# Kernel optimization log

Hardware: AMD Instinct MI355X
Metric: run time of the kernel (lower is better)

Reference implementation:

```python
import jax, jax.numpy as jnp
from jax import lax
import numpy as np

KSIZE = 25  # kernel_size init arg


def _generate_kernel(size):
    center = size // 2
    kernel = np.zeros((size, size), dtype=np.float32)
    for i in range(size):
        if i < center + 1:
            for j in range(size):
                if j < center:
                    kernel[i, j] = j - center - i
                elif j > center:
                    kernel[i, j] = -kernel[i, size - j - 1]
        elif i > center:
            kernel[i, :] = kernel[size - i - 1, :]
    return kernel


def _edge_forward(cube):
    # cube: [B, H, W, C]. Equivalent to the torch block-tiled computation:
    # zero-pad by p, for every interior pixel compute spectral-angle (SAD)
    # between the center spectrum and each pixel of its k x k neighborhood,
    # then 'convolve' (single valid k x k cross-correlation == weighted sum)
    # the SAD patch with fixed gradient kernels Kx / Ky.
    B, H, W, C = cube.shape
    k = KSIZE
    p = k // 2
    Kx = jnp.asarray(_generate_kernel(k))  # [k, k]
    Ky = Kx.T                               # rearrange 'h w -> w h'
    kx_flat = Kx.reshape(-1)
    ky_flat = Ky.reshape(-1)

    padded = jnp.pad(cube, ((0, 0), (p, p), (p, p), (0, 0)))  # [B, H+2p, W+2p, C]
    norm_pad = jnp.sqrt(jnp.sum(padded * padded, axis=-1))    # [B, H+2p, W+2p]
    center = cube                                             # center spectra
    norm_c = norm_pad[:, p:p + H, p:p + W]                    # [B, H, W]

    # Scan over the k*k window offsets; accumulate the two gradient sums
    # without ever materializing the [B,H,W,k,k] SAD volume.
    def step(carry, idx):
        gx, gy = carry
        di, dj = idx // k, idx % k
        shifted = lax.dynamic_slice(padded, (0, di, dj, 0), (B, H, W, C))
        norm_s = lax.dynamic_slice(norm_pad, (0, di, dj), (B, H, W))
        numer = jnp.einsum('bhwc,bhwc->bhw', center, shifted)
        # eps 1e-4 matches torch; tiny clip guards fp32 roundoff past +/-1
        ratio = jnp.clip(numer / (norm_c * norm_s + 1e-4), -1.0 + 1e-6, 1.0 - 1e-6)
        sad = jnp.arccos(ratio)
        return (gx + sad * kx_flat[idx], gy + sad * ky_flat[idx]), None

    init = (jnp.zeros((B, H, W), cube.dtype), jnp.zeros((B, H, W), cube.dtype))
    (gx, gy), _ = lax.scan(jax.checkpoint(step), init, jnp.arange(k * k))
    edge = jnp.abs(gx) + jnp.abs(gy)
    # the torch code zeroes a pad_len border before global-max normalization
    out = jnp.pad(edge[:, p:H - p, p:W - p], ((0, 0), (p, p), (p, p)))
    return out / jnp.max(out)


def setup_inputs() -> dict:
    key = jax.random.key(0)
    cube = jax.random.uniform(key, (1, 400, 400, 128), dtype=jnp.float32)
    return {"cube": cube}


def reference(cube):
    return _edge_forward(cube)
```

## Files before the change

### kernel.cpp

```cpp
#include <hip/hip_runtime.h>
#include <cstdint>
#include <cstddef>


typedef _Float16 half8 __attribute__((ext_vector_type(8)));
typedef float    f32x4 __attribute__((ext_vector_type(4)));

#define HW   400
#define NP   (HW*HW)
#define CCH  128
#define W16  416
#define ROWE (W16*CCH)
#define PAD  12
#define IEND 388
#define LDSF 132


__global__ void cvt_kernel(const float* __restrict__ cube,
                           _Float16* __restrict__ c16,
                           unsigned* __restrict__ gmax) {
  __shared__ float buf[16*LDSF];
  __shared__ float part[16];
  int pg = blockIdx.x;
  int rb = blockIdx.y;
  int t  = threadIdx.x;
  if (pg == 0 && rb == 0 && t == 0) *gmax = 0u;
  int pa = t >> 5, oa = (t & 31)*4;
  int p  = t >> 4, k  = t & 15;
  int i  = t & 15, cb = t >> 4;
  for (int r = rb*10; r < rb*10 + 10; ++r) {
    if (pg == 25) {
      half8 hz;
      #pragma unroll
      for (int j = 0; j < 8; ++j) hz[j] = (_Float16)0.f;
      *(half8*)(c16 + (size_t)r*ROWE + 25*2048 + t*8) = hz;
      continue;
    }
    const float4* src4 = (const float4*)(cube + ((size_t)(r*HW + pg*16))*CCH);
    float4 fa = src4[t];
    float4 fb = src4[t + 256];
    __syncthreads();
    *(float4*)&buf[pa*LDSF + oa]     = fa;
    *(float4*)&buf[(8+pa)*LDSF + oa] = fb;
    __syncthreads();
    const float4* pr = (const float4*)&buf[p*LDSF + k*8];
    float4 x0 = pr[0], x1 = pr[1];
    float ss = x0.x*x0.x + x0.y*x0.y + x0.z*x0.z + x0.w*x0.w
             + x1.x*x1.x + x1.y*x1.y + x1.z*x1.z + x1.w*x1.w;
    ss += __shfl_xor(ss, 1);
    ss += __shfl_xor(ss, 2);
    ss += __shfl_xor(ss, 4);
    ss += __shfl_xor(ss, 8);
    if (k == 0) part[p] = ss;
    __syncthreads();
    float tot = part[i];
    float sc = (tot > 0.f) ? rsqrtf(tot) : 0.f;
    const float4* vp = (const float4*)&buf[i*LDSF + cb*8];
    float4 v0 = vp[0], v1 = vp[1];
    half8 hv;
    hv[0] = (_Float16)(v0.x*sc); hv[1] = (_Float16)(v0.y*sc);
    hv[2] = (_Float16)(v0.z*sc); hv[3] = (_Float16)(v0.w*sc);
    hv[4] = (_Float16)(v1.x*sc); hv[5] = (_Float16)(v1.y*sc);
    hv[6] = (_Float16)(v1.z*sc); hv[7] = (_Float16)(v1.w*sc);
    *(half8*)(c16 + (size_t)r*ROWE + pg*2048 + t*8) = hv;
  }
}

__global__ __launch_bounds__(256) void edge_kernel(
    const _Float16* __restrict__ c16,
    float* __restrict__ gxp, float* __restrict__ gyp) {
  const int id  = blockIdx.x;
  const int g   = (id & 7)*564 + (id >> 3);
  const int row = g / 12;
  const int rem = g - row*12;
  const int half = rem & 1;
  const int wbq  = rem >> 1;
  const int h   = row + PAD;
  const int wv  = threadIdx.x >> 6;
  const int wb  = wbq*4 + wv;
  const int l   = threadIdx.x & 63;
  const int c   = l & 15, q = l >> 4;
  const int w0  = PAD + 16*wb;

  half8 A[4];
  {
    int px = w0 + c;
    const _Float16* pA = c16 + (size_t)h*ROWE + (px >> 4)*2048 + q*128 + (px & 15)*8;
    #pragma unroll
    for (int ks = 0; ks < 4; ++ks)
      A[ks] = *(const half8*)(pA + ks*512);
  }

  const float cq = (float)(c - 4*q);

  float S0[3][4], S1[3][4];
  #pragma unroll
  for (int d = 0; d < 3; ++d)
    #pragma unroll
    for (int rr = 0; rr < 4; ++rr) { S0[d][rr] = 0.f; S1[d][rr] = 0.f; }

  const f32x4 z4 = {0.f, 0.f, 0.f, 0.f};
  const _Float16* bBase = c16 + wb*2048 + (size_t)l*8;
  const int diLo = half ? 12 : 0;
  const int diHi = half ? 25 : 13;

  #pragma unroll 1
  for (int di = diLo; di < diHi; ++di) {
    const int r = h + di - PAD;
    const _Float16* rowB = bBase + (size_t)r*ROWE;

    f32x4 acc[3];

    #pragma unroll
    for (int ks = 0; ks < 4; ++ks) {
      half8 B0 = *(const half8*)(rowB + 0*2048 + ks*512);
      half8 B1 = *(const half8*)(rowB + 1*2048 + ks*512);
      half8 B2 = *(const half8*)(rowB + 2*2048 + ks*512);
      if (ks == 0) {
        acc[0] = __builtin_amdgcn_mfma_f32_16x16x32_f16(A[0], B0, z4, 0,0,0);
        acc[1] = __builtin_amdgcn_mfma_f32_16x16x32_f16(A[0], B1, z4, 0,0,0);
        acc[2] = __builtin_amdgcn_mfma_f32_16x16x32_f16(A[0], B2, z4, 0,0,0);
      } else {
        acc[0] = __builtin_amdgcn_mfma_f32_16x16x32_f16(A[ks], B0, acc[0], 0,0,0);
        acc[1] = __builtin_amdgcn_mfma_f32_16x16x32_f16(A[ks], B1, acc[1], 0,0,0);
        acc[2] = __builtin_amdgcn_mfma_f32_16x16x32_f16(A[ks], B2, acc[2], 0,0,0);
      }
    }

    const float ii  = (float)((di <= 12) ? di : 24 - di);
    const float w0s = (di == 12) ? 0.5f : 1.0f;
    const float w1s = w0s * ii;

    #pragma unroll
    for (int d = 0; d < 3; ++d)
      #pragma unroll
      for (int rr = 0; rr < 4; ++rr) {
        float x  = acc[d][rr];
        float sq = __builtin_amdgcn_sqrtf(fmaxf(1.0f - x, 0.0f));
        float pl = fmaf(x, -0.0187292994f, 0.0742610134f);
        pl = fmaf(pl, x, -0.2121143967f);
        pl = fmaf(pl, x,  1.5707287572f);
        float sad = sq * pl;
        S0[d][rr] = fmaf(sad, w0s, S0[d][rr]);
        S1[d][rr] = fmaf(sad, w1s, S1[d][rr]);
      }
  }

  const float s_h = half ? 1.0f : -1.0f;
  float gx[4], gy[4];
  #pragma unroll
  for (int rr = 0; rr < 4; ++rr) { gx[rr] = 0.f; gy[rr] = 0.f; }

  #pragma unroll
  for (int d = 0; d < 3; ++d)
    #pragma unroll
    for (int rr = 0; rr < 4; ++rr) {
      float p   = cq + (float)(16*d - 12 - rr);
      float ap  = fabsf(p);
      float mnj = 12.0f - ap;
      bool  ok  = mnj >= 0.0f;
      float sg  = fminf(fmaxf(p, -1.0f), 1.0f);
      float wy  = 12.0f + mnj;
      float s0 = S0[d][rr], s1 = S1[d][rr];
      gx[rr] += ok ? fmaf(sg, s1, p*s0) : 0.0f;
      gy[rr] += ok ? s_h*fmaf(wy, s0, -s1) : 0.0f;
    }

  const int hoff = half*NP + h*HW;
  #pragma unroll
  for (int rr = 0; rr < 4; ++rr) {
    float sgx = gx[rr], sgy = gy[rr];
    #pragma unroll
    for (int m = 1; m < 16; m <<= 1) {
      sgx += __shfl_xor(sgx, m);
      sgy += __shfl_xor(sgy, m);
    }
    if (c == rr) {
      int w = w0 + 4*q + rr;
      gxp[hoff + w] = sgx;
      gyp[hoff + w] = sgy;
    }
  }
}

__global__ void combine_kernel(float* __restrict__ gxp,
                               const float* __restrict__ gyp,
                               unsigned* __restrict__ gmax) {
  __shared__ float wm[4];
  int idx = blockIdx.x*256 + threadIdx.x;
  int hh = idx / HW;
  int ww = idx - hh*HW;
  float e = 0.f;
  if (hh >= PAD && hh < IEND && ww >= PAD && ww < IEND)
    e = fabsf(gxp[idx] + gxp[NP + idx]) + fabsf(gyp[idx] + gyp[NP + idx]);
  gxp[idx] = e;
  float m = e;
  #pragma unroll
  for (int off = 1; off < 64; off <<= 1) m = fmaxf(m, __shfl_xor(m, off));
  if ((threadIdx.x & 63) == 0) wm[threadIdx.x >> 6] = m;
  __syncthreads();
  if (threadIdx.x == 0) {
    float mm = fmaxf(fmaxf(wm[0], wm[1]), fmaxf(wm[2], wm[3]));
    atomicMax(gmax, __float_as_uint(mm));
  }
}

__global__ void norm_kernel(const float* __restrict__ edge,
                            const unsigned* __restrict__ gmax,
                            float* __restrict__ out) {
  int idx = blockIdx.x*256 + threadIdx.x;
  float mv = __uint_as_float(*gmax);
  out[idx] = edge[idx] / mv;
}

extern "C" void kernel_launch(void* const* d_in, const int* in_sizes, int n_in,
                              void* d_out, int out_size, void* d_ws, size_t ws_size,
                              hipStream_t stream) {
  const float* cube = (const float*)d_in[0];
  char* ws = (char*)d_ws;
  _Float16* c16  = (_Float16*)(ws);
  float*    gxp  = (float*)(ws + 42598400);
  float*    gyp  = (float*)(ws + 42598400 + 8*NP);
  unsigned* gmax = (unsigned*)(ws + 42598400 + 16*NP);

  cvt_kernel<<<dim3(26, 40), 256, 0, stream>>>(cube, c16, gmax);
  edge_kernel<<<4512, 256, 0, stream>>>(c16, gxp, gyp);
  combine_kernel<<<NP/256, 256, 0, stream>>>(gxp, gyp, gmax);
  norm_kernel<<<NP/256, 256, 0, stream>>>(gxp, gmax, (float*)d_out);
}
```

Measured before the change: 232.7 us.

## Prefetch next row's B fragments and pack SAD math into float2 ops

The edge kernel now loads the B operands for the next neighborhood row into registers right after issuing the current row's MFMAs, so global-load latency overlaps the arccos/accumulate work. The per-element SAD polynomial and accumulation are rewritten with two-wide float vectors so the compiler can emit packed FP32 instructions. The launch bounds also request 4 blocks per CU as a minimum-occupancy hint. The 12 extra prefetched half8 registers raise register pressure, which could lead to spills under the tighter occupancy bound.

```diff
diff --git a/kernel.cpp b/kernel.cpp
--- a/kernel.cpp
+++ b/kernel.cpp
@@ -5,6 +5,7 @@
 
 typedef _Float16 half8 __attribute__((ext_vector_type(8)));
 typedef float    f32x4 __attribute__((ext_vector_type(4)));
+typedef float    f32x2 __attribute__((ext_vector_type(2)));
 
 #define HW   400
 #define NP   (HW*HW)
@@ -66,7 +67,7 @@
   }
 }
 
-__global__ __launch_bounds__(256) void edge_kernel(
+__global__ __launch_bounds__(256, 4) void edge_kernel(
     const _Float16* __restrict__ c16,
     float* __restrict__ gxp, float* __restrict__ gyp) {
   const int id  = blockIdx.x;
@@ -93,56 +94,84 @@
 
   const float cq = (float)(c - 4*q);
 
-  float S0[3][4], S1[3][4];
+  f32x2 S0[3][2], S1[3][2];
   #pragma unroll
   for (int d = 0; d < 3; ++d)
     #pragma unroll
-    for (int rr = 0; rr < 4; ++rr) { S0[d][rr] = 0.f; S1[d][rr] = 0.f; }
+    for (int pp = 0; pp < 2; ++pp) {
+      S0[d][pp] = (f32x2){0.f, 0.f};
+      S1[d][pp] = (f32x2){0.f, 0.f};
+    }
 
   const f32x4 z4 = {0.f, 0.f, 0.f, 0.f};
+  const f32x2 one2  = {1.f, 1.f};
+  const f32x2 zero2 = {0.f, 0.f};
+  const f32x2 pc3 = {-0.0187292994f, -0.0187292994f};
+  const f32x2 pc2 = { 0.0742610134f,  0.0742610134f};
+  const f32x2 pc1 = {-0.2121143967f, -0.2121143967f};
+  const f32x2 pc0 = { 1.5707287572f,  1.5707287572f};
+
   const _Float16* bBase = c16 + wb*2048 + (size_t)l*8;
   const int diLo = half ? 12 : 0;
   const int diHi = half ? 25 : 13;
 
+  half8 B[3][4];
+  {
+    const _Float16* rowB = bBase + (size_t)(h + diLo - PAD)*ROWE;
+    #pragma unroll
+    for (int gg = 0; gg < 3; ++gg)
+      #pragma unroll
+      for (int ks = 0; ks < 4; ++ks)
+        B[gg][ks] = *(const half8*)(rowB + gg*2048 + ks*512);
+  }
+
   #pragma unroll 1
   for (int di = diLo; di < diHi; ++di) {
-    const int r = h + di - PAD;
-    const _Float16* rowB = bBase + (size_t)r*ROWE;
-
     f32x4 acc[3];
-
     #pragma unroll
     for (int ks = 0; ks < 4; ++ks) {
-      half8 B0 = *(const half8*)(rowB + 0*2048 + ks*512);
-      half8 B1 = *(const half8*)(rowB + 1*2048 + ks*512);
-      half8 B2 = *(const half8*)(rowB + 2*2048 + ks*512);
       if (ks == 0) {
-        acc[0] = __builtin_amdgcn_mfma_f32_16x16x32_f16(A[0], B0, z4, 0,0,0);
-        acc[1] = __builtin_amdgcn_mfma_f32_16x16x32_f16(A[0], B1, z4, 0,0,0);
-        acc[2] = __builtin_amdgcn_mfma_f32_16x16x32_f16(A[0], B2, z4, 0,0,0);
+        acc[0] = __builtin_amdgcn_mfma_f32_16x16x32_f16(A[0], B[0][0], z4, 0,0,0);
+        acc[1] = __builtin_amdgcn_mfma_f32_16x16x32_f16(A[0], B[1][0], z4, 0,0,0);
+        acc[2] = __builtin_amdgcn_mfma_f32_16x16x32_f16(A[0], B[2][0], z4, 0,0,0);
       } else {
-        acc[0] = __builtin_amdgcn_mfma_f32_16x16x32_f16(A[ks], B0, acc[0], 0,0,0);
-        acc[1] = __builtin_amdgcn_mfma_f32_16x16x32_f16(A[ks], B1, acc[1], 0,0,0);
-        acc[2] = __builtin_amdgcn_mfma_f32_16x16x32_f16(A[ks], B2, acc[2], 0,0,0);
+        acc[0] = __builtin_amdgcn_mfma_f32_16x16x32_f16(A[ks], B[0][ks], acc[0], 0,0,0);
+        acc[1] = __builtin_amdgcn_mfma_f32_16x16x32_f16(A[ks], B[1][ks], acc[1], 0,0,0);
+        acc[2] = __builtin_amdgcn_mfma_f32_16x16x32_f16(A[ks], B[2][ks], acc[2], 0,0,0);
       }
+    }
+
+    if (di + 1 < diHi) {
+      const _Float16* rowB = bBase + (size_t)(h + di + 1 - PAD)*ROWE;
+      #pragma unroll
+      for (int gg = 0; gg < 3; ++gg)
+        #pragma unroll
+        for (int ks = 0; ks < 4; ++ks)
+          B[gg][ks] = *(const half8*)(rowB + gg*2048 + ks*512);
     }
 
     const float ii  = (float)((di <= 12) ? di : 24 - di);
     const float w0s = (di == 12) ? 0.5f : 1.0f;
     const float w1s = w0s * ii;
+    const f32x2 w0v = {w0s, w0s};
+    const f32x2 w1v = {w1s, w1s};
 
     #pragma unroll
     for (int d = 0; d < 3; ++d)
       #pragma unroll
-      for (int rr = 0; rr < 4; ++rr) {
-        float x  = acc[d][rr];
-        float sq = __builtin_amdgcn_sqrtf(fmaxf(1.0f - x, 0.0f));
-        float pl = fmaf(x, -0.0187292994f, 0.0742610134f);
-        pl = fmaf(pl, x, -0.2121143967f);
-        pl = fmaf(pl, x,  1.5707287572f);
-        float sad = sq * pl;
-        S0[d][rr] = fmaf(sad, w0s, S0[d][rr]);
-        S1[d][rr] = fmaf(sad, w1s, S1[d][rr]);
+      for (int pp = 0; pp < 2; ++pp) {
+        f32x2 x2 = { acc[d][2*pp], acc[d][2*pp + 1] };
+        f32x2 t2 = one2 - x2;
+        t2 = __builtin_elementwise_max(t2, zero2);
+        f32x2 s2;
+        s2.x = __builtin_amdgcn_sqrtf(t2.x);
+        s2.y = __builtin_amdgcn_sqrtf(t2.y);
+        f32x2 p2 = __builtin_elementwise_fma(x2, pc3, pc2);
+        p2 = __builtin_elementwise_fma(p2, x2, pc1);
+        p2 = __builtin_elementwise_fma(p2, x2, pc0);
+        f32x2 sad2 = s2 * p2;
+        S0[d][pp] = __builtin_elementwise_fma(sad2, w0v, S0[d][pp]);
+        S1[d][pp] = __builtin_elementwise_fma(sad2, w1v, S1[d][pp]);
       }
   }
 
@@ -161,7 +190,8 @@
       bool  ok  = mnj >= 0.0f;
       float sg  = fminf(fmaxf(p, -1.0f), 1.0f);
       float wy  = 12.0f + mnj;
-      float s0 = S0[d][rr], s1 = S1[d][rr];
+      float s0 = S0[d][rr >> 1][rr & 1];
+      float s1 = S1[d][rr >> 1][rr & 1];
       gx[rr] += ok ? fmaf(sg, s1, p*s0) : 0.0f;
       gy[rr] += ok ? s_h*fmaf(wy, s0, -s1) : 0.0f;
     }
```

After: 226.4 us. -2.7%, faster.

## Share neighbor rows across 4 output rows via LDS ring buffer in edge kernel

Applied to the files above, without the earlier changes.

Each block now processes four consecutive output rows (one per wave) over the full 25-row window, instead of splitting the window into two halves across blocks. Neighbor rows are staged through a 5-slot LDS ring buffer, prefetched into registers one iteration ahead, so each loaded row is reused by all four waves. This cuts global/L2 traffic and removes the half-partial buffers and their sum in combine. The cost is extra accumulators and register pressure, about 60KB of LDS per block, and a block-wide barrier every iteration.

```diff
diff --git a/kernel.cpp b/kernel.cpp
--- a/kernel.cpp
+++ b/kernel.cpp
@@ -14,6 +14,8 @@
 #define PAD  12
 #define IEND 388
 #define LDSF 132
+#define NSLOT 5
+#define SLOTB 12288
 
 
 __global__ void cvt_kernel(const float* __restrict__ cube,
@@ -69,18 +71,17 @@
 __global__ __launch_bounds__(256) void edge_kernel(
     const _Float16* __restrict__ c16,
     float* __restrict__ gxp, float* __restrict__ gyp) {
-  const int id  = blockIdx.x;
-  const int g   = (id & 7)*564 + (id >> 3);
-  const int row = g / 12;
-  const int rem = g - row*12;
-  const int half = rem & 1;
-  const int wbq  = rem >> 1;
-  const int h   = row + PAD;
-  const int wv  = threadIdx.x >> 6;
-  const int wb  = wbq*4 + wv;
-  const int l   = threadIdx.x & 63;
-  const int c   = l & 15, q = l >> 4;
-  const int w0  = PAD + 16*wb;
+  __shared__ char bs[NSLOT*SLOTB];
+  const int id = blockIdx.x;
+  const int g  = (id & 7)*282 + (id >> 3);
+  const int hq = g / 24;
+  const int wb = g - hq*24;
+  const int h0 = PAD + 4*hq;
+  const int wv = threadIdx.x >> 6;
+  const int h  = h0 + wv;
+  const int l  = threadIdx.x & 63;
+  const int c  = l & 15, q = l >> 4;
+  const int w0 = PAD + 16*wb;
 
   half8 A[4];
   {
@@ -93,29 +94,45 @@
 
   const float cq = (float)(c - 4*q);
 
-  float S0[3][4], S1[3][4];
+  float S0[3][4], S1[3][4], T0[3][4], T1[3][4];
   #pragma unroll
   for (int d = 0; d < 3; ++d)
     #pragma unroll
-    for (int rr = 0; rr < 4; ++rr) { S0[d][rr] = 0.f; S1[d][rr] = 0.f; }
+    for (int rr = 0; rr < 4; ++rr) {
+      S0[d][rr] = 0.f; S1[d][rr] = 0.f; T0[d][rr] = 0.f; T1[d][rr] = 0.f;
+    }
 
   const f32x4 z4 = {0.f, 0.f, 0.f, 0.f};
-  const _Float16* bBase = c16 + wb*2048 + (size_t)l*8;
-  const int diLo = half ? 12 : 0;
-  const int diHi = half ? 25 : 13;
+
+  #pragma unroll
+  for (int s = 0; s < 4; ++s) {
+    const _Float16* src = c16 + (size_t)(h0 - 12 + s)*ROWE + wb*2048
+                        + wv*1536 + (size_t)l*8;
+    char* dst = &bs[s*SLOTB + wv*3072 + l*16];
+    #pragma unroll
+    for (int k = 0; k < 3; ++k)
+      *(half8*)(dst + k*1024) = *(const half8*)(src + k*512);
+  }
+  __syncthreads();
 
   #pragma unroll 1
-  for (int di = diLo; di < diHi; ++di) {
-    const int r = h + di - PAD;
-    const _Float16* rowB = bBase + (size_t)r*ROWE;
-
+  for (int di = 0; di < 25; ++di) {
+    half8 st0, st1, st2;
+    if (di < 24) {
+      const _Float16* src = c16 + (size_t)(h0 + di - 8)*ROWE + wb*2048
+                          + wv*1536 + (size_t)l*8;
+      st0 = *(const half8*)(src);
+      st1 = *(const half8*)(src + 512);
+      st2 = *(const half8*)(src + 1024);
+    }
+
+    const char* bsw = &bs[((di + wv) % NSLOT)*SLOTB];
     f32x4 acc[3];
-
     #pragma unroll
     for (int ks = 0; ks < 4; ++ks) {
-      half8 B0 = *(const half8*)(rowB + 0*2048 + ks*512);
-      half8 B1 = *(const half8*)(rowB + 1*2048 + ks*512);
-      half8 B2 = *(const half8*)(rowB + 2*2048 + ks*512);
+      half8 B0 = *(const half8*)(bsw + 0*4096 + ks*1024 + l*16);
+      half8 B1 = *(const half8*)(bsw + 1*4096 + ks*1024 + l*16);
+      half8 B2 = *(const half8*)(bsw + 2*4096 + ks*1024 + l*16);
       if (ks == 0) {
         acc[0] = __builtin_amdgcn_mfma_f32_16x16x32_f16(A[0], B0, z4, 0,0,0);
         acc[1] = __builtin_amdgcn_mfma_f32_16x16x32_f16(A[0], B1, z4, 0,0,0);
@@ -128,8 +145,8 @@
     }
 
     const float ii  = (float)((di <= 12) ? di : 24 - di);
-    const float w0s = (di == 12) ? 0.5f : 1.0f;
-    const float w1s = w0s * ii;
+    const float sdi = (float)((di > 12) - (di < 12));
+    const float wt1 = sdi * ii;
 
     #pragma unroll
     for (int d = 0; d < 3; ++d)
@@ -141,12 +158,21 @@
         pl = fmaf(pl, x, -0.2121143967f);
         pl = fmaf(pl, x,  1.5707287572f);
         float sad = sq * pl;
-        S0[d][rr] = fmaf(sad, w0s, S0[d][rr]);
-        S1[d][rr] = fmaf(sad, w1s, S1[d][rr]);
+        S0[d][rr] += sad;
+        S1[d][rr] = fmaf(sad, ii,  S1[d][rr]);
+        T0[d][rr] = fmaf(sad, sdi, T0[d][rr]);
+        T1[d][rr] = fmaf(sad, wt1, T1[d][rr]);
       }
-  }
-
-  const float s_h = half ? 1.0f : -1.0f;
+
+    if (di < 24) {
+      char* dst = &bs[((di + 4) % NSLOT)*SLOTB + wv*3072 + l*16];
+      *(half8*)(dst)        = st0;
+      *(half8*)(dst + 1024) = st1;
+      *(half8*)(dst + 2048) = st2;
+    }
+    __syncthreads();
+  }
+
   float gx[4], gy[4];
   #pragma unroll
   for (int rr = 0; rr < 4; ++rr) { gx[rr] = 0.f; gy[rr] = 0.f; }
@@ -161,12 +187,11 @@
       bool  ok  = mnj >= 0.0f;
       float sg  = fminf(fmaxf(p, -1.0f), 1.0f);
       float wy  = 12.0f + mnj;
-      float s0 = S0[d][rr], s1 = S1[d][rr];
-      gx[rr] += ok ? fmaf(sg, s1, p*s0) : 0.0f;
-      gy[rr] += ok ? s_h*fmaf(wy, s0, -s1) : 0.0f;
-    }
-
-  const int hoff = half*NP + h*HW;
+      gx[rr] += ok ? fmaf(sg, S1[d][rr], p*S0[d][rr]) : 0.0f;
+      gy[rr] += ok ? fmaf(wy, T0[d][rr], -T1[d][rr]) : 0.0f;
+    }
+
+  const int hoff = h*HW;
   #pragma unroll
   for (int rr = 0; rr < 4; ++rr) {
     float sgx = gx[rr], sgy = gy[rr];
@@ -192,7 +217,7 @@
   int ww = idx - hh*HW;
   float e = 0.f;
   if (hh >= PAD && hh < IEND && ww >= PAD && ww < IEND)
-    e = fabsf(gxp[idx] + gxp[NP + idx]) + fabsf(gyp[idx] + gyp[NP + idx]);
+    e = fabsf(gxp[idx]) + fabsf(gyp[idx]);
   gxp[idx] = e;
   float m = e;
   #pragma unroll
@@ -220,11 +245,11 @@
   char* ws = (char*)d_ws;
   _Float16* c16  = (_Float16*)(ws);
   float*    gxp  = (float*)(ws + 42598400);
-  float*    gyp  = (float*)(ws + 42598400 + 8*NP);
-  unsigned* gmax = (unsigned*)(ws + 42598400 + 16*NP);
+  float*    gyp  = (float*)(ws + 42598400 + 4*NP);
+  unsigned* gmax = (unsigned*)(ws + 42598400 + 8*NP);
 
   cvt_kernel<<<dim3(26, 40), 256, 0, stream>>>(cube, c16, gmax);
-  edge_kernel<<<4512, 256, 0, stream>>>(c16, gxp, gyp);
+  edge_kernel<<<2256, 256, 0, stream>>>(c16, gxp, gyp);
   combine_kernel<<<NP/256, 256, 0, stream>>>(gxp, gyp, gmax);
   norm_kernel<<<NP/256, 256, 0, stream>>>(gxp, gmax, (float*)d_out);
 }
```

New measurement: 233.5 us. No clear change (+0.3%).
